# Kernel optimization log

Hardware: AMD Instinct MI355X
Metric: run time of the kernel (lower is better)

## Reference

```python
import jax, jax.numpy as jnp
import numpy as np

N_NODES = 100000
N_EDGES = 1600000
D_FEAT = 48


def sage_conv(x, src, dst, Wl, Wr, b):
    # mean aggregation of neighbor messages x[src] at dst (PyG source_to_target)
    msg_sum = jax.ops.segment_sum(x[src], dst, num_segments=N_NODES)  # [N, d]
    cnt = jax.ops.segment_sum(jnp.ones((src.shape[0],), x.dtype), dst,
                              num_segments=N_NODES)  # [N]
    mean = msg_sum / jnp.maximum(cnt, 1.0)[:, None]
    # out = lin_l(mean neighbors) + lin_r(self); bias only on lin_l (PyG default)
    return mean @ Wl + b + x @ Wr


def setup_inputs() -> dict:
    key = jax.random.key(0)
    ks = jax.random.split(key, 8)
    x = jax.random.normal(ks[0], (N_NODES, D_FEAT), jnp.float32)
    edge_index = jax.random.randint(ks[1], (2, N_EDGES), 0, N_NODES, jnp.int64)
    def w(k, fi, fo):
        return jax.random.normal(k, (fi, fo), jnp.float32) / np.sqrt(fi)
    return {
        "x": x,
        "edge_index": edge_index,
        "W1l": w(ks[2], D_FEAT, 32), "W1r": w(ks[3], D_FEAT, 32),
        "b1": jnp.zeros((32,), jnp.float32),
        "W2l": w(ks[4], 32, 16), "W2r": w(ks[5], 32, 16),
        "b2": jnp.zeros((16,), jnp.float32),
        "Wlin": w(ks[6], 16, 2), "blin": jnp.zeros((2,), jnp.float32),
    }


def reference(x, edge_index, W1l, W1r, b1, W2l, W2r, b2, Wlin, blin):
    src, dst = edge_index[0], edge_index[1]
    h = jax.nn.relu(sage_conv(x, src, dst, W1l, W1r, b1))
    h = jax.nn.relu(sage_conv(h, src, dst, W2l, W2r, b2))
    return h @ Wlin + blin  # [N, 2] logits
```

## Files before the change

kernel.cpp:

```cpp
#include <hip/hip_runtime.h>
#include <hip/hip_bf16.h>


constexpr int NN  = 100000;
constexpr int NE  = 1600000;
constexpr int NCH = (NN + 255) / 256;
constexpr int NB  = 391;
constexpr int CAP = 4608;
constexpr int SEG = CAP + 3 * 256;
constexpr int T1  = 2048;
constexpr int NB1 = (NE + T1 - 1) / T1;

__device__ __forceinline__ float bl(unsigned u) { return __uint_as_float(u << 16); }
__device__ __forceinline__ float bh(unsigned u) { return __uint_as_float(u & 0xffff0000u); }
__device__ __forceinline__ unsigned f2b(float x) {
    unsigned u = __float_as_uint(x);
    return (u + 0x7fffu + ((u >> 16) & 1u)) >> 16;
}
__device__ __forceinline__ unsigned pack2(float a, float b) {
    return f2b(a) | (f2b(b) << 16);
}

__device__ __forceinline__ int wave_incl_scan(int v, int lane) {
#pragma unroll
    for (int d = 1; d < 64; d <<= 1) {
        int t = __shfl_up(v, d, 64);
        if (lane >= d) v += t;
    }
    return v;
}

__global__ __launch_bounds__(256) void k1_kernel(
    const float* __restrict__ X,
    const float* __restrict__ Wl,
    const float* __restrict__ Wr,
    const int*   __restrict__ ei,
    int* __restrict__ bsize, unsigned* __restrict__ bbuf,
    __hip_bfloat16* __restrict__ P, __hip_bfloat16* __restrict__ R)
{
    __shared__ float sW[2][48 * 32];
    __shared__ int hist[NB], base[NB];
    __shared__ int s_any;

    if (blockIdx.x < NCH) {
        for (int i = threadIdx.x; i < 48 * 32; i += 256) {
            sW[0][i] = Wl[i];
            sW[1][i] = Wr[i];
        }
        __syncthreads();
        int n = blockIdx.x * 256 + threadIdx.x;
        if (n > NN) return;
        if (n == NN) {
            uint4 z = make_uint4(0, 0, 0, 0);
            uint4* pp = reinterpret_cast<uint4*>(P + (size_t)NN * 32);
#pragma unroll
            for (int i = 0; i < 4; ++i) pp[i] = z;
            return;
        }
        float xr[48];
        const float4* xp = reinterpret_cast<const float4*>(X + (size_t)n * 48);
#pragma unroll
        for (int i = 0; i < 12; ++i) {
            float4 u = xp[i];
            xr[i*4+0] = u.x; xr[i*4+1] = u.y; xr[i*4+2] = u.z; xr[i*4+3] = u.w;
        }
        float accp[32], accr[32];
#pragma unroll
        for (int j = 0; j < 32; ++j) { accp[j] = 0.f; accr[j] = 0.f; }
#pragma unroll
        for (int k = 0; k < 48; ++k) {
            float xk = xr[k];
#pragma unroll
            for (int j = 0; j < 32; ++j) {
                accp[j] += xk * sW[0][k * 32 + j];
                accr[j] += xk * sW[1][k * 32 + j];
            }
        }
        uint4* pp = reinterpret_cast<uint4*>(P + (size_t)n * 32);
        uint4* rp = reinterpret_cast<uint4*>(R + (size_t)n * 32);
#pragma unroll
        for (int i = 0; i < 4; ++i) {
            uint4 u, v;
            u.x = pack2(accp[i*8+0], accp[i*8+1]); u.y = pack2(accp[i*8+2], accp[i*8+3]);
            u.z = pack2(accp[i*8+4], accp[i*8+5]); u.w = pack2(accp[i*8+6], accp[i*8+7]);
            v.x = pack2(accr[i*8+0], accr[i*8+1]); v.y = pack2(accr[i*8+2], accr[i*8+3]);
            v.z = pack2(accr[i*8+4], accr[i*8+5]); v.w = pack2(accr[i*8+6], accr[i*8+7]);
            pp[i] = u;
            rp[i] = v;
        }
    } else {
        if (threadIdx.x == 0) s_any = 0;
        for (int i = threadIdx.x; i < NB; i += 256) hist[i] = 0;
        __syncthreads();
        int dv = 0;
        for (int i = threadIdx.x; i < 2048; i += 256) dv |= ei[2 * i + 1];
        if (dv != 0) atomicOr(&s_any, 1);
        __syncthreads();
        const bool i64 = (s_any == 0);
        const int e0 = (blockIdx.x - NCH) * T1;

        auto sweep = [&](auto&& f) {
            if (i64) {
                const int4* sp = reinterpret_cast<const int4*>(ei) + (e0 >> 1);
                const int4* dp = reinterpret_cast<const int4*>(ei) + ((NE + e0) >> 1);
#pragma unroll
                for (int it = 0; it < 4; ++it) {
                    int p = it * 256 + threadIdx.x;
                    int e = e0 + 2 * p;
                    if (e + 2 <= NE) {
                        int4 s4 = sp[p], d4 = dp[p];
                        f(s4.x, d4.x);
                        f(s4.z, d4.z);
                    } else {
                        for (int e2 = e; e2 < NE && e2 < e + 2; ++e2)
                            f(ei[(size_t)e2 << 1], ei[(size_t)(NE + e2) << 1]);
                    }
                }
            } else {
                const int4* sp = reinterpret_cast<const int4*>(ei) + (e0 >> 2);
                const int4* dp = reinterpret_cast<const int4*>(ei) + ((NE + e0) >> 2);
#pragma unroll
                for (int it = 0; it < 2; ++it) {
                    int q = it * 256 + threadIdx.x;
                    int e = e0 + 4 * q;
                    if (e + 4 <= NE) {
                        int4 s4 = sp[q], d4 = dp[q];
                        f(s4.x, d4.x);
                        f(s4.y, d4.y);
                        f(s4.z, d4.z);
                        f(s4.w, d4.w);
                    } else {
                        for (int e2 = e; e2 < NE && e2 < e + 4; ++e2)
                            f(ei[e2], ei[NE + e2]);
                    }
                }
            }
        };

        sweep([&](int s, int d) {
            if ((unsigned)s < (unsigned)NN && (unsigned)d < (unsigned)NN)
                atomicAdd(&hist[d >> 8], 1);
        });
        __syncthreads();
        for (int b = threadIdx.x; b < NB; b += 256) {
            int h = hist[b];
            base[b] = h ? atomicAdd(&bsize[b], h) : 0;
        }
        __syncthreads();
        sweep([&](int s, int d) {
            if ((unsigned)s < (unsigned)NN && (unsigned)d < (unsigned)NN) {
                int bk = d >> 8;
                int pos = atomicAdd(&base[bk], 1);
                if (pos < CAP)
                    bbuf[(size_t)bk * CAP + pos] =
                        ((unsigned)s << 8) | (unsigned)(d & 255);
            }
        });
    }
}

__global__ __launch_bounds__(1024) void k2_kernel(
    const int* __restrict__ bsize, const unsigned* __restrict__ bbuf,
    int* __restrict__ deg, int* __restrict__ rowstart, int* __restrict__ csr_src)
{
    __shared__ int ldeg[256], lcur[256], ws[4];
    int b = blockIdx.x, t = threadIdx.x;
    int bs = b * SEG;

    int S = min(bsize[b], CAP);
    const unsigned* bp = bbuf + (size_t)b * CAP;
    if (t < 256) ldeg[t] = 0;
    __syncthreads();
    for (int i = t; i < S; i += 1024)
        atomicAdd(&ldeg[bp[i] & 255u], 1);
    __syncthreads();

    int v = 0, pv = 0, incl = 0, excl = 0;
    if (t < 256) {
        v  = ldeg[t];
        pv = (v + 3) & ~3;
        incl = wave_incl_scan(pv, t & 63);
        if ((t & 63) == 63) ws[t >> 6] = incl;
    }
    __syncthreads();
    if (t < 256) {
        int off = 0, wid = t >> 6;
#pragma unroll
        for (int w = 0; w < 3; ++w)
            if (wid > w) off += ws[w];
        excl = off + incl - pv;
        int node = (b << 8) + t;
        if (node < NN) {
            deg[node] = v;
            rowstart[node] = bs + excl;
        }
        lcur[t] = excl;
    }
    __syncthreads();

    for (int i = t; i < S; i += 1024) {
        unsigned pk = bp[i];
        int pos = atomicAdd(&lcur[pk & 255u], 1);
        csr_src[bs + pos] = (int)(pk >> 8);
    }
    if (t < 256)
        for (int p = excl + v; p < excl + pv; ++p)
            csr_src[bs + p] = NN;
}

__global__ __launch_bounds__(256) void gather1f_kernel(
    const int* __restrict__ rowstart, const int* __restrict__ deg,
    const int* __restrict__ csr_src,
    const __hip_bfloat16* __restrict__ p1,
    const __hip_bfloat16* __restrict__ r1,
    const float* __restrict__ b1,
    const float* __restrict__ W2l,
    const float* __restrict__ W2r,
    __hip_bfloat16* __restrict__ P2,
    __hip_bfloat16* __restrict__ R2)
{
    __shared__ float sW2l[32 * 16], sW2r[32 * 16], sb1[32];
    __shared__ float shh[32 * 65];
    int t = threadIdx.x;
    for (int i = t; i < 32 * 16; i += 256) { sW2l[i] = W2l[i]; sW2r[i] = W2r[i]; }
    if (t < 32) sb1[t] = b1[t];
    __syncthreads();

    int loc = t >> 2, c = t & 3;
    int n = blockIdx.x * 64 + loc;
    bool valid = n < NN;

    if (valid) {
        int start = rowstart[n], dn = deg[n];
        int pv4 = ((dn + 3) & ~3) >> 2;
        const uint4* prow = reinterpret_cast<const uint4*>(p1);
        const int4* cp4 = reinterpret_cast<const int4*>(csr_src + start);
        uint4 r = reinterpret_cast<const uint4*>(r1)[(size_t)n * 4 + c];
        float acc[8];
#pragma unroll
        for (int j = 0; j < 8; ++j) acc[j] = 0.f;
        int k = 0;
        int4 sA = cp4[0];
        int4 sB = cp4[1];
        for (; k + 1 < pv4; k += 2) {
            int4 nA = cp4[k + 2];
            int4 nB = cp4[k + 3];
            uint4 a = prow[(size_t)sA.x * 4 + c];
            uint4 b = prow[(size_t)sA.y * 4 + c];
            uint4 d = prow[(size_t)sA.z * 4 + c];
            uint4 e = prow[(size_t)sA.w * 4 + c];
            uint4 f = prow[(size_t)sB.x * 4 + c];
            uint4 g = prow[(size_t)sB.y * 4 + c];
            uint4 h = prow[(size_t)sB.z * 4 + c];
            uint4 m = prow[(size_t)sB.w * 4 + c];
            acc[0] += bl(a.x) + bl(b.x) + bl(d.x) + bl(e.x)
                    + bl(f.x) + bl(g.x) + bl(h.x) + bl(m.x);
            acc[1] += bh(a.x) + bh(b.x) + bh(d.x) + bh(e.x)
                    + bh(f.x) + bh(g.x) + bh(h.x) + bh(m.x);
            acc[2] += bl(a.y) + bl(b.y) + bl(d.y) + bl(e.y)
                    + bl(f.y) + bl(g.y) + bl(h.y) + bl(m.y);
            acc[3] += bh(a.y) + bh(b.y) + bh(d.y) + bh(e.y)
                    + bh(f.y) + bh(g.y) + bh(h.y) + bh(m.y);
            acc[4] += bl(a.z) + bl(b.z) + bl(d.z) + bl(e.z)
                    + bl(f.z) + bl(g.z) + bl(h.z) + bl(m.z);
            acc[5] += bh(a.z) + bh(b.z) + bh(d.z) + bh(e.z)
                    + bh(f.z) + bh(g.z) + bh(h.z) + bh(m.z);
            acc[6] += bl(a.w) + bl(b.w) + bl(d.w) + bl(e.w)
                    + bl(f.w) + bl(g.w) + bl(h.w) + bl(m.w);
            acc[7] += bh(a.w) + bh(b.w) + bh(d.w) + bh(e.w)
                    + bh(f.w) + bh(g.w) + bh(h.w) + bh(m.w);
            sA = nA; sB = nB;
        }
        if (k < pv4) {
            uint4 a = prow[(size_t)sA.x * 4 + c];
            uint4 b = prow[(size_t)sA.y * 4 + c];
            uint4 d = prow[(size_t)sA.z * 4 + c];
            uint4 e = prow[(size_t)sA.w * 4 + c];
            acc[0] += bl(a.x) + bl(b.x) + bl(d.x) + bl(e.x);
            acc[1] += bh(a.x) + bh(b.x) + bh(d.x) + bh(e.x);
            acc[2] += bl(a.y) + bl(b.y) + bl(d.y) + bl(e.y);
            acc[3] += bh(a.y) + bh(b.y) + bh(d.y) + bh(e.y);
            acc[4] += bl(a.z) + bl(b.z) + bl(d.z) + bl(e.z);
            acc[5] += bh(a.z) + bh(b.z) + bh(d.z) + bh(e.z);
            acc[6] += bl(a.w) + bl(b.w) + bl(d.w) + bl(e.w);
            acc[7] += bh(a.w) + bh(b.w) + bh(d.w) + bh(e.w);
        }
        float inv = 1.0f / fmaxf((float)dn, 1.0f);
        float rr[8] = { bl(r.x), bh(r.x), bl(r.y), bh(r.y),
                        bl(r.z), bh(r.z), bl(r.w), bh(r.w) };
#pragma unroll
        for (int j = 0; j < 8; ++j)
            shh[(c * 8 + j) * 65 + loc] = fmaxf(acc[j] * inv + rr[j] + sb1[c * 8 + j], 0.f);
    }
    __syncthreads();

    if (valid) {
        float accp[4], accr[4];
#pragma unroll
        for (int j = 0; j < 4; ++j) { accp[j] = 0.f; accr[j] = 0.f; }
#pragma unroll
        for (int k2i = 0; k2i < 32; ++k2i) {
            float hk = shh[k2i * 65 + loc];
#pragma unroll
            for (int j = 0; j < 4; ++j) {
                accp[j] += hk * sW2l[k2i * 16 + c * 4 + j];
                accr[j] += hk * sW2r[k2i * 16 + c * 4 + j];
            }
        }
        uint2 up, ur;
        up.x = pack2(accp[0], accp[1]); up.y = pack2(accp[2], accp[3]);
        ur.x = pack2(accr[0], accr[1]); ur.y = pack2(accr[2], accr[3]);
        reinterpret_cast<uint2*>(P2)[(size_t)n * 4 + c] = up;
        reinterpret_cast<uint2*>(R2)[(size_t)n * 4 + c] = ur;
    } else if (n == NN) {
        uint2 z = make_uint2(0, 0);
        reinterpret_cast<uint2*>(P2)[(size_t)NN * 4 + c] = z;
        reinterpret_cast<uint2*>(R2)[(size_t)NN * 4 + c] = z;
    }
}

__global__ __launch_bounds__(256) void gather2_kernel(
    const int* __restrict__ rowstart, const int* __restrict__ deg,
    const int* __restrict__ csr_src,
    const __hip_bfloat16* __restrict__ P2,
    const __hip_bfloat16* __restrict__ R2,
    const float* __restrict__ b2,
    const float* __restrict__ Wlin,
    const float* __restrict__ blin,
    float* __restrict__ out)
{
    __shared__ float sb[16], sW[32], sbl[2];
    if (threadIdx.x < 16) sb[threadIdx.x] = b2[threadIdx.x];
    else if (threadIdx.x < 48) sW[threadIdx.x - 16] = Wlin[threadIdx.x - 16];
    else if (threadIdx.x < 50) sbl[threadIdx.x - 48] = blin[threadIdx.x - 48];
    __syncthreads();
    int t = blockIdx.x * 256 + threadIdx.x;
    int n = t >> 1, c = t & 1;
    if (n >= NN) return;
    int start = rowstart[n], dn = deg[n];
    int pv4 = ((dn + 3) & ~3) >> 2;

    const uint4* prow = reinterpret_cast<const uint4*>(P2);
    const int4* cp4 = reinterpret_cast<const int4*>(csr_src + start);
    uint4 r = reinterpret_cast<const uint4*>(R2)[(size_t)n * 2 + c];
    float acc[8];
#pragma unroll
    for (int j = 0; j < 8; ++j) acc[j] = 0.f;
    int k = 0;
    int4 sA = cp4[0];
    int4 sB = cp4[1];
    for (; k + 1 < pv4; k += 2) {
        int4 nA = cp4[k + 2];
        int4 nB = cp4[k + 3];
        uint4 a = prow[(size_t)sA.x * 2 + c];
        uint4 b = prow[(size_t)sA.y * 2 + c];
        uint4 d = prow[(size_t)sA.z * 2 + c];
        uint4 e = prow[(size_t)sA.w * 2 + c];
        uint4 f = prow[(size_t)sB.x * 2 + c];
        uint4 g = prow[(size_t)sB.y * 2 + c];
        uint4 h = prow[(size_t)sB.z * 2 + c];
        uint4 m = prow[(size_t)sB.w * 2 + c];
        acc[0] += bl(a.x) + bl(b.x) + bl(d.x) + bl(e.x)
                + bl(f.x) + bl(g.x) + bl(h.x) + bl(m.x);
        acc[1] += bh(a.x) + bh(b.x) + bh(d.x) + bh(e.x)
                + bh(f.x) + bh(g.x) + bh(h.x) + bh(m.x);
        acc[2] += bl(a.y) + bl(b.y) + bl(d.y) + bl(e.y)
                + bl(f.y) + bl(g.y) + bl(h.y) + bl(m.y);
        acc[3] += bh(a.y) + bh(b.y) + bh(d.y) + bh(e.y)
                + bh(f.y) + bh(g.y) + bh(h.y) + bh(m.y);
        acc[4] += bl(a.z) + bl(b.z) + bl(d.z) + bl(e.z)
                + bl(f.z) + bl(g.z) + bl(h.z) + bl(m.z);
        acc[5] += bh(a.z) + bh(b.z) + bh(d.z) + bh(e.z)
                + bh(f.z) + bh(g.z) + bh(h.z) + bh(m.z);
        acc[6] += bl(a.w) + bl(b.w) + bl(d.w) + bl(e.w)
                + bl(f.w) + bl(g.w) + bl(h.w) + bl(m.w);
        acc[7] += bh(a.w) + bh(b.w) + bh(d.w) + bh(e.w)
                + bh(f.w) + bh(g.w) + bh(h.w) + bh(m.w);
        sA = nA; sB = nB;
    }
    if (k < pv4) {
        uint4 a = prow[(size_t)sA.x * 2 + c];
        uint4 b = prow[(size_t)sA.y * 2 + c];
        uint4 d = prow[(size_t)sA.z * 2 + c];
        uint4 e = prow[(size_t)sA.w * 2 + c];
        acc[0] += bl(a.x) + bl(b.x) + bl(d.x) + bl(e.x);
        acc[1] += bh(a.x) + bh(b.x) + bh(d.x) + bh(e.x);
        acc[2] += bl(a.y) + bl(b.y) + bl(d.y) + bl(e.y);
        acc[3] += bh(a.y) + bh(b.y) + bh(d.y) + bh(e.y);
        acc[4] += bl(a.z) + bl(b.z) + bl(d.z) + bl(e.z);
        acc[5] += bh(a.z) + bh(b.z) + bh(d.z) + bh(e.z);
        acc[6] += bl(a.w) + bl(b.w) + bl(d.w) + bl(e.w);
        acc[7] += bh(a.w) + bh(b.w) + bh(d.w) + bh(e.w);
    }
    float inv = 1.0f / fmaxf((float)dn, 1.0f);
    float rr[8] = { bl(r.x), bh(r.x), bl(r.y), bh(r.y),
                    bl(r.z), bh(r.z), bl(r.w), bh(r.w) };
    float o0 = 0.f, o1 = 0.f;
#pragma unroll
    for (int j = 0; j < 8; ++j) {
        int kk = c * 8 + j;
        float hv = fmaxf(acc[j] * inv + rr[j] + sb[kk], 0.f);
        o0 += hv * sW[kk * 2];
        o1 += hv * sW[kk * 2 + 1];
    }
    o0 += __shfl_xor(o0, 1, 64);
    o1 += __shfl_xor(o1, 1, 64);
    if (c == 0)
        reinterpret_cast<float2*>(out)[n] = make_float2(o0 + sbl[0], o1 + sbl[1]);
}

extern "C" void kernel_launch(void* const* d_in, const int* in_sizes, int n_in,
                              void* d_out, int out_size, void* d_ws, size_t ws_size,
                              hipStream_t stream)
{
    const float* x    = (const float*)d_in[0];
    const int*   ei   = (const int*)d_in[1];
    const float* W1l  = (const float*)d_in[2];
    const float* W1r  = (const float*)d_in[3];
    const float* b1   = (const float*)d_in[4];
    const float* W2l  = (const float*)d_in[5];
    const float* W2r  = (const float*)d_in[6];
    const float* b2   = (const float*)d_in[7];
    const float* Wlin = (const float*)d_in[8];
    const float* blin = (const float*)d_in[9];
    float* out = (float*)d_out;

    char* wsb = (char*)d_ws;
    int*      bsize    = (int*)(wsb + 64);
    int*      deg      = (int*)(wsb + 4096);
    int*      rowstart = (int*)(wsb + 404096);
    int*      csr_src  = (int*)(wsb + 804096);
    unsigned* bbuf     = (unsigned*)(wsb + 9300000);
    __hip_bfloat16* p1 = (__hip_bfloat16*)(wsb + 16600000);
    __hip_bfloat16* r1 = (__hip_bfloat16*)(wsb + 23100000);
    __hip_bfloat16* p2 = (__hip_bfloat16*)(wsb + 29600000);
    __hip_bfloat16* r2 = (__hip_bfloat16*)(wsb + 32900000);

    dim3 blk(256);

    hipMemsetAsync(bsize, 0, NB * sizeof(int), stream);
    k1_kernel<<<NCH + NB1, blk, 0, stream>>>(x, W1l, W1r, ei, bsize, bbuf, p1, r1);
    k2_kernel<<<NB, dim3(1024), 0, stream>>>(bsize, bbuf, deg, rowstart, csr_src);
    gather1f_kernel<<<(NN + 1 + 63) / 64, blk, 0, stream>>>(
        rowstart, deg, csr_src, p1, r1, b1, W2l, W2r, p2, r2);
    gather2_kernel<<<(NN * 2 + 255) / 256, blk, 0, stream>>>(
        rowstart, deg, csr_src, p2, r2, b2, Wlin, blin, out);
}
```

Baseline: 175.9 us.

## Fuse CSR build into both gather kernels using shared-memory per-bucket CSR

Removes the separate k2 CSR-construction kernel and the global deg/rowstart/csr_src arrays. Each gather block now rebuilds its bucket's CSR in LDS from the bucketed edge buffer. Layer 1 uses half-buckets of 128 nodes per 512-thread block; layer 2 uses full 256-node buckets. This saves one launch and the global CSR write/read traffic. In exchange, the bucket is scanned twice (layer 2 reads it again and layer 1 filters each half), blocks are larger and use more LDS, and there are fewer blocks, which may lower occupancy for the latency-bound gathers.

```diff
diff --git a/kernel.cpp b/kernel.cpp
--- a/kernel.cpp
+++ b/kernel.cpp
@@ -8,6 +8,7 @@
 constexpr int NB  = 391;
 constexpr int CAP = 4608;
 constexpr int SEG = CAP + 3 * 256;
+constexpr int HSEG = CAP + 3 * 128;
 constexpr int T1  = 2048;
 constexpr int NB1 = (NE + T1 - 1) / T1;
 
@@ -159,58 +160,8 @@
     }
 }
 
-__global__ __launch_bounds__(1024) void k2_kernel(
+__global__ __launch_bounds__(512) void kg1_kernel(
     const int* __restrict__ bsize, const unsigned* __restrict__ bbuf,
-    int* __restrict__ deg, int* __restrict__ rowstart, int* __restrict__ csr_src)
-{
-    __shared__ int ldeg[256], lcur[256], ws[4];
-    int b = blockIdx.x, t = threadIdx.x;
-    int bs = b * SEG;
-
-    int S = min(bsize[b], CAP);
-    const unsigned* bp = bbuf + (size_t)b * CAP;
-    if (t < 256) ldeg[t] = 0;
-    __syncthreads();
-    for (int i = t; i < S; i += 1024)
-        atomicAdd(&ldeg[bp[i] & 255u], 1);
-    __syncthreads();
-
-    int v = 0, pv = 0, incl = 0, excl = 0;
-    if (t < 256) {
-        v  = ldeg[t];
-        pv = (v + 3) & ~3;
-        incl = wave_incl_scan(pv, t & 63);
-        if ((t & 63) == 63) ws[t >> 6] = incl;
-    }
-    __syncthreads();
-    if (t < 256) {
-        int off = 0, wid = t >> 6;
-#pragma unroll
-        for (int w = 0; w < 3; ++w)
-            if (wid > w) off += ws[w];
-        excl = off + incl - pv;
-        int node = (b << 8) + t;
-        if (node < NN) {
-            deg[node] = v;
-            rowstart[node] = bs + excl;
-        }
-        lcur[t] = excl;
-    }
-    __syncthreads();
-
-    for (int i = t; i < S; i += 1024) {
-        unsigned pk = bp[i];
-        int pos = atomicAdd(&lcur[pk & 255u], 1);
-        csr_src[bs + pos] = (int)(pk >> 8);
-    }
-    if (t < 256)
-        for (int p = excl + v; p < excl + pv; ++p)
-            csr_src[bs + p] = NN;
-}
-
-__global__ __launch_bounds__(256) void gather1f_kernel(
-    const int* __restrict__ rowstart, const int* __restrict__ deg,
-    const int* __restrict__ csr_src,
     const __hip_bfloat16* __restrict__ p1,
     const __hip_bfloat16* __restrict__ r1,
     const float* __restrict__ b1,
@@ -219,22 +170,66 @@
     __hip_bfloat16* __restrict__ P2,
     __hip_bfloat16* __restrict__ R2)
 {
+    __shared__ alignas(16) int csr[HSEG + 8];
+    __shared__ int ldeg[128], lcur[128], ws[2];
     __shared__ float sW2l[32 * 16], sW2r[32 * 16], sb1[32];
-    __shared__ float shh[32 * 65];
+    __shared__ float shh[32 * 129];
+
     int t = threadIdx.x;
-    for (int i = t; i < 32 * 16; i += 256) { sW2l[i] = W2l[i]; sW2r[i] = W2r[i]; }
+    int b = blockIdx.x >> 1, h = blockIdx.x & 1;
+
+    sW2l[t] = W2l[t];
+    sW2r[t] = W2r[t];
     if (t < 32) sb1[t] = b1[t];
+    if (t < 128) ldeg[t] = 0;
+    __syncthreads();
+
+    int S = min(bsize[b], CAP);
+    const unsigned* bp = bbuf + (size_t)b * CAP;
+    for (int i = t; i < S; i += 512) {
+        unsigned pk = bp[i];
+        int ln = pk & 255u;
+        if ((ln >> 7) == h) atomicAdd(&ldeg[ln & 127], 1);
+    }
+    __syncthreads();
+
+    int v = 0, pv = 0, incl = 0, excl = 0;
+    if (t < 128) {
+        v  = ldeg[t];
+        pv = (v + 3) & ~3;
+        incl = wave_incl_scan(pv, t & 63);
+        if ((t & 63) == 63) ws[t >> 6] = incl;
+    }
+    __syncthreads();
+    if (t < 128) {
+        int off = (t >> 6) ? ws[0] : 0;
+        excl = off + incl - pv;
+        lcur[t] = excl;
+    }
+    __syncthreads();
+    for (int i = t; i < S; i += 512) {
+        unsigned pk = bp[i];
+        int ln = pk & 255u;
+        if ((ln >> 7) == h) {
+            int pos = atomicAdd(&lcur[ln & 127], 1);
+            csr[pos] = (int)(pk >> 8);
+        }
+    }
+    if (t < 128)
+        for (int p = excl + v; p < excl + pv; ++p)
+            csr[p] = NN;
     __syncthreads();
 
     int loc = t >> 2, c = t & 3;
-    int n = blockIdx.x * 64 + loc;
+    int n = (b << 8) + (h << 7) + loc;
     bool valid = n < NN;
 
     if (valid) {
-        int start = rowstart[n], dn = deg[n];
+        int dn = ldeg[loc];
+        int start = lcur[loc] - dn;
         int pv4 = ((dn + 3) & ~3) >> 2;
         const uint4* prow = reinterpret_cast<const uint4*>(p1);
-        const int4* cp4 = reinterpret_cast<const int4*>(csr_src + start);
+        const int4* cp4 = reinterpret_cast<const int4*>(csr + start);
         uint4 r = reinterpret_cast<const uint4*>(r1)[(size_t)n * 4 + c];
         float acc[8];
 #pragma unroll
@@ -246,51 +241,51 @@
             int4 nA = cp4[k + 2];
             int4 nB = cp4[k + 3];
             uint4 a = prow[(size_t)sA.x * 4 + c];
-            uint4 b = prow[(size_t)sA.y * 4 + c];
+            uint4 bq = prow[(size_t)sA.y * 4 + c];
             uint4 d = prow[(size_t)sA.z * 4 + c];
             uint4 e = prow[(size_t)sA.w * 4 + c];
             uint4 f = prow[(size_t)sB.x * 4 + c];
             uint4 g = prow[(size_t)sB.y * 4 + c];
-            uint4 h = prow[(size_t)sB.z * 4 + c];
+            uint4 hq = prow[(size_t)sB.z * 4 + c];
             uint4 m = prow[(size_t)sB.w * 4 + c];
-            acc[0] += bl(a.x) + bl(b.x) + bl(d.x) + bl(e.x)
-                    + bl(f.x) + bl(g.x) + bl(h.x) + bl(m.x);
-            acc[1] += bh(a.x) + bh(b.x) + bh(d.x) + bh(e.x)
-                    + bh(f.x) + bh(g.x) + bh(h.x) + bh(m.x);
-            acc[2] += bl(a.y) + bl(b.y) + bl(d.y) + bl(e.y)
-                    + bl(f.y) + bl(g.y) + bl(h.y) + bl(m.y);
-            acc[3] += bh(a.y) + bh(b.y) + bh(d.y) + bh(e.y)
-                    + bh(f.y) + bh(g.y) + bh(h.y) + bh(m.y);
-            acc[4] += bl(a.z) + bl(b.z) + bl(d.z) + bl(e.z)
-                    + bl(f.z) + bl(g.z) + bl(h.z) + bl(m.z);
-            acc[5] += bh(a.z) + bh(b.z) + bh(d.z) + bh(e.z)
-                    + bh(f.z) + bh(g.z) + bh(h.z) + bh(m.z);
-            acc[6] += bl(a.w) + bl(b.w) + bl(d.w) + bl(e.w)
-                    + bl(f.w) + bl(g.w) + bl(h.w) + bl(m.w);
-            acc[7] += bh(a.w) + bh(b.w) + bh(d.w) + bh(e.w)
-                    + bh(f.w) + bh(g.w) + bh(h.w) + bh(m.w);
+            acc[0] += bl(a.x) + bl(bq.x) + bl(d.x) + bl(e.x)
+                    + bl(f.x) + bl(g.x) + bl(hq.x) + bl(m.x);
+            acc[1] += bh(a.x) + bh(bq.x) + bh(d.x) + bh(e.x)
+                    + bh(f.x) + bh(g.x) + bh(hq.x) + bh(m.x);
+            acc[2] += bl(a.y) + bl(bq.y) + bl(d.y) + bl(e.y)
+                    + bl(f.y) + bl(g.y) + bl(hq.y) + bl(m.y);
+            acc[3] += bh(a.y) + bh(bq.y) + bh(d.y) + bh(e.y)
+                    + bh(f.y) + bh(g.y) + bh(hq.y) + bh(m.y);
+            acc[4] += bl(a.z) + bl(bq.z) + bl(d.z) + bl(e.z)
+                    + bl(f.z) + bl(g.z) + bl(hq.z) + bl(m.z);
+            acc[5] += bh(a.z) + bh(bq.z) + bh(d.z) + bh(e.z)
+                    + bh(f.z) + bh(g.z) + bh(hq.z) + bh(m.z);
+            acc[6] += bl(a.w) + bl(bq.w) + bl(d.w) + bl(e.w)
+                    + bl(f.w) + bl(g.w) + bl(hq.w) + bl(m.w);
+            acc[7] += bh(a.w) + bh(bq.w) + bh(d.w) + bh(e.w)
+                    + bh(f.w) + bh(g.w) + bh(hq.w) + bh(m.w);
             sA = nA; sB = nB;
         }
         if (k < pv4) {
             uint4 a = prow[(size_t)sA.x * 4 + c];
-            uint4 b = prow[(size_t)sA.y * 4 + c];
+            uint4 bq = prow[(size_t)sA.y * 4 + c];
             uint4 d = prow[(size_t)sA.z * 4 + c];
             uint4 e = prow[(size_t)sA.w * 4 + c];
-            acc[0] += bl(a.x) + bl(b.x) + bl(d.x) + bl(e.x);
-            acc[1] += bh(a.x) + bh(b.x) + bh(d.x) + bh(e.x);
-            acc[2] += bl(a.y) + bl(b.y) + bl(d.y) + bl(e.y);
-            acc[3] += bh(a.y) + bh(b.y) + bh(d.y) + bh(e.y);
-            acc[4] += bl(a.z) + bl(b.z) + bl(d.z) + bl(e.z);
-            acc[5] += bh(a.z) + bh(b.z) + bh(d.z) + bh(e.z);
-            acc[6] += bl(a.w) + bl(b.w) + bl(d.w) + bl(e.w);
-            acc[7] += bh(a.w) + bh(b.w) + bh(d.w) + bh(e.w);
+            acc[0] += bl(a.x) + bl(bq.x) + bl(d.x) + bl(e.x);
+            acc[1] += bh(a.x) + bh(bq.x) + bh(d.x) + bh(e.x);
+            acc[2] += bl(a.y) + bl(bq.y) + bl(d.y) + bl(e.y);
+            acc[3] += bh(a.y) + bh(bq.y) + bh(d.y) + bh(e.y);
+            acc[4] += bl(a.z) + bl(bq.z) + bl(d.z) + bl(e.z);
+            acc[5] += bh(a.z) + bh(bq.z) + bh(d.z) + bh(e.z);
+            acc[6] += bl(a.w) + bl(bq.w) + bl(d.w) + bl(e.w);
+            acc[7] += bh(a.w) + bh(bq.w) + bh(d.w) + bh(e.w);
         }
         float inv = 1.0f / fmaxf((float)dn, 1.0f);
         float rr[8] = { bl(r.x), bh(r.x), bl(r.y), bh(r.y),
                         bl(r.z), bh(r.z), bl(r.w), bh(r.w) };
 #pragma unroll
         for (int j = 0; j < 8; ++j)
-            shh[(c * 8 + j) * 65 + loc] = fmaxf(acc[j] * inv + rr[j] + sb1[c * 8 + j], 0.f);
+            shh[(c * 8 + j) * 129 + loc] = fmaxf(acc[j] * inv + rr[j] + sb1[c * 8 + j], 0.f);
     }
     __syncthreads();
 
@@ -300,7 +295,7 @@
         for (int j = 0; j < 4; ++j) { accp[j] = 0.f; accr[j] = 0.f; }
 #pragma unroll
         for (int k2i = 0; k2i < 32; ++k2i) {
-            float hk = shh[k2i * 65 + loc];
+            float hk = shh[k2i * 129 + loc];
 #pragma unroll
             for (int j = 0; j < 4; ++j) {
                 accp[j] += hk * sW2l[k2i * 16 + c * 4 + j];
@@ -319,9 +314,8 @@
     }
 }
 
-__global__ __launch_bounds__(256) void gather2_kernel(
-    const int* __restrict__ rowstart, const int* __restrict__ deg,
-    const int* __restrict__ csr_src,
+__global__ __launch_bounds__(512) void kg2_kernel(
+    const int* __restrict__ bsize, const unsigned* __restrict__ bbuf,
     const __hip_bfloat16* __restrict__ P2,
     const __hip_bfloat16* __restrict__ R2,
     const float* __restrict__ b2,
@@ -329,19 +323,59 @@
     const float* __restrict__ blin,
     float* __restrict__ out)
 {
+    __shared__ alignas(16) int csr[SEG + 8];
+    __shared__ int ldeg[256], lcur[256], ws[4];
     __shared__ float sb[16], sW[32], sbl[2];
-    if (threadIdx.x < 16) sb[threadIdx.x] = b2[threadIdx.x];
-    else if (threadIdx.x < 48) sW[threadIdx.x - 16] = Wlin[threadIdx.x - 16];
-    else if (threadIdx.x < 50) sbl[threadIdx.x - 48] = blin[threadIdx.x - 48];
-    __syncthreads();
-    int t = blockIdx.x * 256 + threadIdx.x;
-    int n = t >> 1, c = t & 1;
+
+    int t = threadIdx.x, b = blockIdx.x;
+    if (t < 16) sb[t] = b2[t];
+    else if (t < 48) sW[t - 16] = Wlin[t - 16];
+    else if (t < 50) sbl[t - 48] = blin[t - 48];
+    if (t < 256) ldeg[t] = 0;
+    __syncthreads();
+
+    int S = min(bsize[b], CAP);
+    const unsigned* bp = bbuf + (size_t)b * CAP;
+    for (int i = t; i < S; i += 512)
+        atomicAdd(&ldeg[bp[i] & 255u], 1);
+    __syncthreads();
+
+    int v = 0, pv = 0, incl = 0, excl = 0;
+    if (t < 256) {
+        v  = ldeg[t];
+        pv = (v + 3) & ~3;
+        incl = wave_incl_scan(pv, t & 63);
+        if ((t & 63) == 63) ws[t >> 6] = incl;
+    }
+    __syncthreads();
+    if (t < 256) {
+        int off = 0, wid = t >> 6;
+#pragma unroll
+        for (int w = 0; w < 3; ++w)
+            if (wid > w) off += ws[w];
+        excl = off + incl - pv;
+        lcur[t] = excl;
+    }
+    __syncthreads();
+    for (int i = t; i < S; i += 512) {
+        unsigned pk = bp[i];
+        int pos = atomicAdd(&lcur[pk & 255u], 1);
+        csr[pos] = (int)(pk >> 8);
+    }
+    if (t < 256)
+        for (int p = excl + v; p < excl + pv; ++p)
+            csr[p] = NN;
+    __syncthreads();
+
+    int ln = t >> 1, c = t & 1;
+    int n = (b << 8) + ln;
     if (n >= NN) return;
-    int start = rowstart[n], dn = deg[n];
+    int dn = ldeg[ln];
+    int start = lcur[ln] - dn;
     int pv4 = ((dn + 3) & ~3) >> 2;
 
     const uint4* prow = reinterpret_cast<const uint4*>(P2);
-    const int4* cp4 = reinterpret_cast<const int4*>(csr_src + start);
+    const int4* cp4 = reinterpret_cast<const int4*>(csr + start);
     uint4 r = reinterpret_cast<const uint4*>(R2)[(size_t)n * 2 + c];
     float acc[8];
 #pragma unroll
@@ -353,44 +387,44 @@
         int4 nA = cp4[k + 2];
         int4 nB = cp4[k + 3];
         uint4 a = prow[(size_t)sA.x * 2 + c];
-        uint4 b = prow[(size_t)sA.y * 2 + c];
+        uint4 bq = prow[(size_t)sA.y * 2 + c];
         uint4 d = prow[(size_t)sA.z * 2 + c];
         uint4 e = prow[(size_t)sA.w * 2 + c];
         uint4 f = prow[(size_t)sB.x * 2 + c];
         uint4 g = prow[(size_t)sB.y * 2 + c];
         uint4 h = prow[(size_t)sB.z * 2 + c];
         uint4 m = prow[(size_t)sB.w * 2 + c];
-        acc[0] += bl(a.x) + bl(b.x) + bl(d.x) + bl(e.x)
+        acc[0] += bl(a.x) + bl(bq.x) + bl(d.x) + bl(e.x)
                 + bl(f.x) + bl(g.x) + bl(h.x) + bl(m.x);
-        acc[1] += bh(a.x) + bh(b.x) + bh(d.x) + bh(e.x)
+        acc[1] += bh(a.x) + bh(bq.x) + bh(d.x) + bh(e.x)
                 + bh(f.x) + bh(g.x) + bh(h.x) + bh(m.x);
-        acc[2] += bl(a.y) + bl(b.y) + bl(d.y) + bl(e.y)
+        acc[2] += bl(a.y) + bl(bq.y) + bl(d.y) + bl(e.y)
                 + bl(f.y) + bl(g.y) + bl(h.y) + bl(m.y);
-        acc[3] += bh(a.y) + bh(b.y) + bh(d.y) + bh(e.y)
+        acc[3] += bh(a.y) + bh(bq.y) + bh(d.y) + bh(e.y)
                 + bh(f.y) + bh(g.y) + bh(h.y) + bh(m.y);
-        acc[4] += bl(a.z) + bl(b.z) + bl(d.z) + bl(e.z)
+        acc[4] += bl(a.z) + bl(bq.z) + bl(d.z) + bl(e.z)
                 + bl(f.z) + bl(g.z) + bl(h.z) + bl(m.z);
-        acc[5] += bh(a.z) + bh(b.z) + bh(d.z) + bh(e.z)
+        acc[5] += bh(a.z) + bh(bq.z) + bh(d.z) + bh(e.z)
                 + bh(f.z) + bh(g.z) + bh(h.z) + bh(m.z);
-        acc[6] += bl(a.w) + bl(b.w) + bl(d.w) + bl(e.w)
+        acc[6] += bl(a.w) + bl(bq.w) + bl(d.w) + bl(e.w)
                 + bl(f.w) + bl(g.w) + bl(h.w) + bl(m.w);
-        acc[7] += bh(a.w) + bh(b.w) + bh(d.w) + bh(e.w)
+        acc[7] += bh(a.w) + bh(bq.w) + bh(d.w) + bh(e.w)
                 + bh(f.w) + bh(g.w) + bh(h.w) + bh(m.w);
         sA = nA; sB = nB;
     }
     if (k < pv4) {
         uint4 a = prow[(size_t)sA.x * 2 + c];
-        uint4 b = prow[(size_t)sA.y * 2 + c];
+        uint4 bq = prow[(size_t)sA.y * 2 + c];
         uint4 d = prow[(size_t)sA.z * 2 + c];
         uint4 e = prow[(size_t)sA.w * 2 + c];
-        acc[0] += bl(a.x) + bl(b.x) + bl(d.x) + bl(e.x);
-        acc[1] += bh(a.x) + bh(b.x) + bh(d.x) + bh(e.x);
-        acc[2] += bl(a.y) + bl(b.y) + bl(d.y) + bl(e.y);
-        acc[3] += bh(a.y) + bh(b.y) + bh(d.y) + bh(e.y);
-        acc[4] += bl(a.z) + bl(b.z) + bl(d.z) + bl(e.z);
-        acc[5] += bh(a.z) + bh(b.z) + bh(d.z) + bh(e.z);
-        acc[6] += bl(a.w) + bl(b.w) + bl(d.w) + bl(e.w);
-        acc[7] += bh(a.w) + bh(b.w) + bh(d.w) + bh(e.w);
+        acc[0] += bl(a.x) + bl(bq.x) + bl(d.x) + bl(e.x);
+        acc[1] += bh(a.x) + bh(bq.x) + bh(d.x) + bh(e.x);
+        acc[2] += bl(a.y) + bl(bq.y) + bl(d.y) + bl(e.y);
+        acc[3] += bh(a.y) + bh(bq.y) + bh(d.y) + bh(e.y);
+        acc[4] += bl(a.z) + bl(bq.z) + bl(d.z) + bl(e.z);
+        acc[5] += bh(a.z) + bh(bq.z) + bh(d.z) + bh(e.z);
+        acc[6] += bl(a.w) + bl(bq.w) + bl(d.w) + bl(e.w);
+        acc[7] += bh(a.w) + bh(bq.w) + bh(d.w) + bh(e.w);
     }
     float inv = 1.0f / fmaxf((float)dn, 1.0f);
     float rr[8] = { bl(r.x), bh(r.x), bl(r.y), bh(r.y),
@@ -427,9 +461,6 @@
 
     char* wsb = (char*)d_ws;
     int*      bsize    = (int*)(wsb + 64);
-    int*      deg      = (int*)(wsb + 4096);
-    int*      rowstart = (int*)(wsb + 404096);
-    int*      csr_src  = (int*)(wsb + 804096);
     unsigned* bbuf     = (unsigned*)(wsb + 9300000);
     __hip_bfloat16* p1 = (__hip_bfloat16*)(wsb + 16600000);
     __hip_bfloat16* r1 = (__hip_bfloat16*)(wsb + 23100000);
@@ -440,9 +471,8 @@
 
     hipMemsetAsync(bsize, 0, NB * sizeof(int), stream);
     k1_kernel<<<NCH + NB1, blk, 0, stream>>>(x, W1l, W1r, ei, bsize, bbuf, p1, r1);
-    k2_kernel<<<NB, dim3(1024), 0, stream>>>(bsize, bbuf, deg, rowstart, csr_src);
-    gather1f_kernel<<<(NN + 1 + 63) / 64, blk, 0, stream>>>(
-        rowstart, deg, csr_src, p1, r1, b1, W2l, W2r, p2, r2);
-    gather2_kernel<<<(NN * 2 + 255) / 256, blk, 0, stream>>>(
-        rowstart, deg, csr_src, p2, r2, b2, Wlin, blin, out);
-}
+    kg1_kernel<<<NB * 2, dim3(512), 0, stream>>>(
+        bsize, bbuf, p1, r1, b1, W2l, W2r, p2, r2);
+    kg2_kernel<<<NB, dim3(512), 0, stream>>>(
+        bsize, bbuf, p2, r2, b2, Wlin, blin, out);
+}
```

After: 177.5 us. About the same (+0.9%).

## Fuse CSR bucket build with layer-1 gather and split first-layer linear by weight

Applied to the files above, without the earlier changes.

The CSR construction kernel is merged with the layer-1 gather. Each 1024-thread block builds its 256-node segment's CSR in shared memory, gathers neighbors from it directly, and still writes the CSR out for layer 2. This removes one launch and a global round-trip of the CSR before gather 1. Separately, the first linear kernel now assigns Wl and Wr projections to different blocks, halving per-thread registers and doubling block count. The risks are only 391 large blocks in the fused kernel, which limits parallelism during the latency-bound gather, and heavy shared memory use.

```diff
diff --git a/kernel.cpp b/kernel.cpp
--- a/kernel.cpp
+++ b/kernel.cpp
@@ -4,7 +4,7 @@
 
 constexpr int NN  = 100000;
 constexpr int NE  = 1600000;
-constexpr int NCH = (NN + 255) / 256;
+constexpr int NLN = 391;
 constexpr int NB  = 391;
 constexpr int CAP = 4608;
 constexpr int SEG = CAP + 3 * 256;
@@ -38,23 +38,26 @@
     int* __restrict__ bsize, unsigned* __restrict__ bbuf,
     __hip_bfloat16* __restrict__ P, __hip_bfloat16* __restrict__ R)
 {
-    __shared__ float sW[2][48 * 32];
+    __shared__ float sW1[48 * 32];
     __shared__ int hist[NB], base[NB];
     __shared__ int s_any;
 
-    if (blockIdx.x < NCH) {
-        for (int i = threadIdx.x; i < 48 * 32; i += 256) {
-            sW[0][i] = Wl[i];
-            sW[1][i] = Wr[i];
-        }
+    if (blockIdx.x < 2 * NLN) {
+        const bool isP = blockIdx.x < NLN;
+        const float* W = isP ? Wl : Wr;
+        __hip_bfloat16* O = isP ? P : R;
+        for (int i = threadIdx.x; i < 48 * 32; i += 256)
+            sW1[i] = W[i];
         __syncthreads();
-        int n = blockIdx.x * 256 + threadIdx.x;
+        int n = (blockIdx.x - (isP ? 0 : NLN)) * 256 + threadIdx.x;
         if (n > NN) return;
         if (n == NN) {
-            uint4 z = make_uint4(0, 0, 0, 0);
-            uint4* pp = reinterpret_cast<uint4*>(P + (size_t)NN * 32);
-#pragma unroll
-            for (int i = 0; i < 4; ++i) pp[i] = z;
+            if (isP) {
+                uint4 z = make_uint4(0, 0, 0, 0);
+                uint4* pp = reinterpret_cast<uint4*>(P + (size_t)NN * 32);
+#pragma unroll
+                for (int i = 0; i < 4; ++i) pp[i] = z;
+            }
             return;
         }
         float xr[48];
@@ -64,29 +67,23 @@
             float4 u = xp[i];
             xr[i*4+0] = u.x; xr[i*4+1] = u.y; xr[i*4+2] = u.z; xr[i*4+3] = u.w;
         }
-        float accp[32], accr[32];
-#pragma unroll
-        for (int j = 0; j < 32; ++j) { accp[j] = 0.f; accr[j] = 0.f; }
+        float acc[32];
+#pragma unroll
+        for (int j = 0; j < 32; ++j) acc[j] = 0.f;
 #pragma unroll
         for (int k = 0; k < 48; ++k) {
             float xk = xr[k];
 #pragma unroll
-            for (int j = 0; j < 32; ++j) {
-                accp[j] += xk * sW[0][k * 32 + j];
-                accr[j] += xk * sW[1][k * 32 + j];
-            }
-        }
-        uint4* pp = reinterpret_cast<uint4*>(P + (size_t)n * 32);
-        uint4* rp = reinterpret_cast<uint4*>(R + (size_t)n * 32);
+            for (int j = 0; j < 32; ++j)
+                acc[j] += xk * sW1[k * 32 + j];
+        }
+        uint4* op = reinterpret_cast<uint4*>(O + (size_t)n * 32);
 #pragma unroll
         for (int i = 0; i < 4; ++i) {
-            uint4 u, v;
-            u.x = pack2(accp[i*8+0], accp[i*8+1]); u.y = pack2(accp[i*8+2], accp[i*8+3]);
-            u.z = pack2(accp[i*8+4], accp[i*8+5]); u.w = pack2(accp[i*8+6], accp[i*8+7]);
-            v.x = pack2(accr[i*8+0], accr[i*8+1]); v.y = pack2(accr[i*8+2], accr[i*8+3]);
-            v.z = pack2(accr[i*8+4], accr[i*8+5]); v.w = pack2(accr[i*8+6], accr[i*8+7]);
-            pp[i] = u;
-            rp[i] = v;
+            uint4 u;
+            u.x = pack2(acc[i*8+0], acc[i*8+1]); u.y = pack2(acc[i*8+2], acc[i*8+3]);
+            u.z = pack2(acc[i*8+4], acc[i*8+5]); u.w = pack2(acc[i*8+6], acc[i*8+7]);
+            op[i] = u;
         }
     } else {
         if (threadIdx.x == 0) s_any = 0;
@@ -97,7 +94,7 @@
         if (dv != 0) atomicOr(&s_any, 1);
         __syncthreads();
         const bool i64 = (s_any == 0);
-        const int e0 = (blockIdx.x - NCH) * T1;
+        const int e0 = (blockIdx.x - 2 * NLN) * T1;
 
         auto sweep = [&](auto&& f) {
             if (i64) {
@@ -159,18 +156,32 @@
     }
 }
 
-__global__ __launch_bounds__(1024) void k2_kernel(
+__global__ __launch_bounds__(1024) void kg1_kernel(
     const int* __restrict__ bsize, const unsigned* __restrict__ bbuf,
-    int* __restrict__ deg, int* __restrict__ rowstart, int* __restrict__ csr_src)
+    const __hip_bfloat16* __restrict__ p1,
+    const __hip_bfloat16* __restrict__ r1,
+    const float* __restrict__ b1,
+    const float* __restrict__ W2l,
+    const float* __restrict__ W2r,
+    int* __restrict__ csr_g,
+    int* __restrict__ deg_g,
+    int* __restrict__ rows_g,
+    __hip_bfloat16* __restrict__ P2,
+    __hip_bfloat16* __restrict__ R2)
 {
+    __shared__ alignas(16) int csr[SEG + 8];
     __shared__ int ldeg[256], lcur[256], ws[4];
-    int b = blockIdx.x, t = threadIdx.x;
-    int bs = b * SEG;
+    __shared__ float sW2l[32 * 16], sW2r[32 * 16], sb1[32];
+    __shared__ float shh[32 * 257];
+
+    int t = threadIdx.x, b = blockIdx.x;
+    if (t < 512) { sW2l[t] = W2l[t]; sW2r[t] = W2r[t]; }
+    else if (t < 544) sb1[t - 512] = b1[t - 512];
+    if (t < 256) ldeg[t] = 0;
+    __syncthreads();
 
     int S = min(bsize[b], CAP);
     const unsigned* bp = bbuf + (size_t)b * CAP;
-    if (t < 256) ldeg[t] = 0;
-    __syncthreads();
     for (int i = t; i < S; i += 1024)
         atomicAdd(&ldeg[bp[i] & 255u], 1);
     __syncthreads();
@@ -189,52 +200,35 @@
         for (int w = 0; w < 3; ++w)
             if (wid > w) off += ws[w];
         excl = off + incl - pv;
+        lcur[t] = excl;
         int node = (b << 8) + t;
         if (node < NN) {
-            deg[node] = v;
-            rowstart[node] = bs + excl;
-        }
-        lcur[t] = excl;
-    }
-    __syncthreads();
-
+            deg_g[node] = v;
+            rows_g[node] = b * SEG + excl;
+        }
+    }
+    __syncthreads();
     for (int i = t; i < S; i += 1024) {
         unsigned pk = bp[i];
         int pos = atomicAdd(&lcur[pk & 255u], 1);
-        csr_src[bs + pos] = (int)(pk >> 8);
+        csr[pos] = (int)(pk >> 8);
     }
     if (t < 256)
         for (int p = excl + v; p < excl + pv; ++p)
-            csr_src[bs + p] = NN;
-}
-
-__global__ __launch_bounds__(256) void gather1f_kernel(
-    const int* __restrict__ rowstart, const int* __restrict__ deg,
-    const int* __restrict__ csr_src,
-    const __hip_bfloat16* __restrict__ p1,
-    const __hip_bfloat16* __restrict__ r1,
-    const float* __restrict__ b1,
-    const float* __restrict__ W2l,
-    const float* __restrict__ W2r,
-    __hip_bfloat16* __restrict__ P2,
-    __hip_bfloat16* __restrict__ R2)
-{
-    __shared__ float sW2l[32 * 16], sW2r[32 * 16], sb1[32];
-    __shared__ float shh[32 * 65];
-    int t = threadIdx.x;
-    for (int i = t; i < 32 * 16; i += 256) { sW2l[i] = W2l[i]; sW2r[i] = W2r[i]; }
-    if (t < 32) sb1[t] = b1[t];
-    __syncthreads();
+            csr[p] = NN;
+    __syncthreads();
+
+    for (int p = t; p < SEG; p += 1024)
+        csr_g[b * SEG + p] = csr[p];
 
     int loc = t >> 2, c = t & 3;
-    int n = blockIdx.x * 64 + loc;
-    bool valid = n < NN;
-
-    if (valid) {
-        int start = rowstart[n], dn = deg[n];
+    int n = (b << 8) + loc;
+    if (n < NN) {
+        int dn = ldeg[loc];
+        int start = lcur[loc] - dn;
         int pv4 = ((dn + 3) & ~3) >> 2;
         const uint4* prow = reinterpret_cast<const uint4*>(p1);
-        const int4* cp4 = reinterpret_cast<const int4*>(csr_src + start);
+        const int4* cp4 = reinterpret_cast<const int4*>(csr + start);
         uint4 r = reinterpret_cast<const uint4*>(r1)[(size_t)n * 4 + c];
         float acc[8];
 #pragma unroll
@@ -246,61 +240,66 @@
             int4 nA = cp4[k + 2];
             int4 nB = cp4[k + 3];
             uint4 a = prow[(size_t)sA.x * 4 + c];
-            uint4 b = prow[(size_t)sA.y * 4 + c];
+            uint4 bq = prow[(size_t)sA.y * 4 + c];
             uint4 d = prow[(size_t)sA.z * 4 + c];
             uint4 e = prow[(size_t)sA.w * 4 + c];
             uint4 f = prow[(size_t)sB.x * 4 + c];
             uint4 g = prow[(size_t)sB.y * 4 + c];
-            uint4 h = prow[(size_t)sB.z * 4 + c];
+            uint4 hq = prow[(size_t)sB.z * 4 + c];
             uint4 m = prow[(size_t)sB.w * 4 + c];
-            acc[0] += bl(a.x) + bl(b.x) + bl(d.x) + bl(e.x)
-                    + bl(f.x) + bl(g.x) + bl(h.x) + bl(m.x);
-            acc[1] += bh(a.x) + bh(b.x) + bh(d.x) + bh(e.x)
-                    + bh(f.x) + bh(g.x) + bh(h.x) + bh(m.x);
-            acc[2] += bl(a.y) + bl(b.y) + bl(d.y) + bl(e.y)
-                    + bl(f.y) + bl(g.y) + bl(h.y) + bl(m.y);
-            acc[3] += bh(a.y) + bh(b.y) + bh(d.y) + bh(e.y)
-                    + bh(f.y) + bh(g.y) + bh(h.y) + bh(m.y);
-            acc[4] += bl(a.z) + bl(b.z) + bl(d.z) + bl(e.z)
-                    + bl(f.z) + bl(g.z) + bl(h.z) + bl(m.z);
-            acc[5] += bh(a.z) + bh(b.z) + bh(d.z) + bh(e.z)
-                    + bh(f.z) + bh(g.z) + bh(h.z) + bh(m.z);
-            acc[6] += bl(a.w) + bl(b.w) + bl(d.w) + bl(e.w)
-                    + bl(f.w) + bl(g.w) + bl(h.w) + bl(m.w);
-            acc[7] += bh(a.w) + bh(b.w) + bh(d.w) + bh(e.w)
-                    + bh(f.w) + bh(g.w) + bh(h.w) + bh(m.w);
+            acc[0] += bl(a.x) + bl(bq.x) + bl(d.x) + bl(e.x)
+                    + bl(f.x) + bl(g.x) + bl(hq.x) + bl(m.x);
+            acc[1] += bh(a.x) + bh(bq.x) + bh(d.x) + bh(e.x)
+                    + bh(f.x) + bh(g.x) + bh(hq.x) + bh(m.x);
+            acc[2] += bl(a.y) + bl(bq.y) + bl(d.y) + bl(e.y)
+                    + bl(f.y) + bl(g.y) + bl(hq.y) + bl(m.y);
+            acc[3] += bh(a.y) + bh(bq.y) + bh(d.y) + bh(e.y)
+                    + bh(f.y) + bh(g.y) + bh(hq.y) + bh(m.y);
+            acc[4] += bl(a.z) + bl(bq.z) + bl(d.z) + bl(e.z)
+                    + bl(f.z) + bl(g.z) + bl(hq.z) + bl(m.z);
+            acc[5] += bh(a.z) + bh(bq.z) + bh(d.z) + bh(e.z)
+                    + bh(f.z) + bh(g.z) + bh(hq.z) + bh(m.z);
+            acc[6] += bl(a.w) + bl(bq.w) + bl(d.w) + bl(e.w)
+                    + bl(f.w) + bl(g.w) + bl(hq.w) + bl(m.w);
+            acc[7] += bh(a.w) + bh(bq.w) + bh(d.w) + bh(e.w)
+                    + bh(f.w) + bh(g.w) + bh(hq.w) + bh(m.w);
             sA = nA; sB = nB;
         }
         if (k < pv4) {
             uint4 a = prow[(size_t)sA.x * 4 + c];
-            uint4 b = prow[(size_t)sA.y * 4 + c];
+            uint4 bq = prow[(size_t)sA.y * 4 + c];
             uint4 d = prow[(size_t)sA.z * 4 + c];
             uint4 e = prow[(size_t)sA.w * 4 + c];
-            acc[0] += bl(a.x) + bl(b.x) + bl(d.x) + bl(e.x);
-            acc[1] += bh(a.x) + bh(b.x) + bh(d.x) + bh(e.x);
-            acc[2] += bl(a.y) + bl(b.y) + bl(d.y) + bl(e.y);
-            acc[3] += bh(a.y) + bh(b.y) + bh(d.y) + bh(e.y);
-            acc[4] += bl(a.z) + bl(b.z) + bl(d.z) + bl(e.z);
-            acc[5] += bh(a.z) + bh(b.z) + bh(d.z) + bh(e.z);
-            acc[6] += bl(a.w) + bl(b.w) + bl(d.w) + bl(e.w);
-            acc[7] += bh(a.w) + bh(b.w) + bh(d.w) + bh(e.w);
+            acc[0] += bl(a.x) + bl(bq.x) + bl(d.x) + bl(e.x);
+            acc[1] += bh(a.x) + bh(bq.x) + bh(d.x) + bh(e.x);
+            acc[2] += bl(a.y) + bl(bq.y) + bl(d.y) + bl(e.y);
+            acc[3] += bh(a.y) + bh(bq.y) + bh(d.y) + bh(e.y);
+            acc[4] += bl(a.z) + bl(bq.z) + bl(d.z) + bl(e.z);
+            acc[5] += bh(a.z) + bh(bq.z) + bh(d.z) + bh(e.z);
+            acc[6] += bl(a.w) + bl(bq.w) + bl(d.w) + bl(e.w);
+            acc[7] += bh(a.w) + bh(bq.w) + bh(d.w) + bh(e.w);
         }
         float inv = 1.0f / fmaxf((float)dn, 1.0f);
         float rr[8] = { bl(r.x), bh(r.x), bl(r.y), bh(r.y),
                         bl(r.z), bh(r.z), bl(r.w), bh(r.w) };
 #pragma unroll
         for (int j = 0; j < 8; ++j)
-            shh[(c * 8 + j) * 65 + loc] = fmaxf(acc[j] * inv + rr[j] + sb1[c * 8 + j], 0.f);
-    }
-    __syncthreads();
-
-    if (valid) {
+            shh[(c * 8 + j) * 257 + loc] =
+                fmaxf(acc[j] * inv + rr[j] + sb1[c * 8 + j], 0.f);
+    } else if (n == NN) {
+        uint2 z = make_uint2(0, 0);
+        reinterpret_cast<uint2*>(P2)[(size_t)NN * 4 + c] = z;
+        reinterpret_cast<uint2*>(R2)[(size_t)NN * 4 + c] = z;
+    }
+    __syncthreads();
+
+    if (n < NN) {
         float accp[4], accr[4];
 #pragma unroll
         for (int j = 0; j < 4; ++j) { accp[j] = 0.f; accr[j] = 0.f; }
 #pragma unroll
         for (int k2i = 0; k2i < 32; ++k2i) {
-            float hk = shh[k2i * 65 + loc];
+            float hk = shh[k2i * 257 + loc];
 #pragma unroll
             for (int j = 0; j < 4; ++j) {
                 accp[j] += hk * sW2l[k2i * 16 + c * 4 + j];
@@ -312,10 +311,6 @@
         ur.x = pack2(accr[0], accr[1]); ur.y = pack2(accr[2], accr[3]);
         reinterpret_cast<uint2*>(P2)[(size_t)n * 4 + c] = up;
         reinterpret_cast<uint2*>(R2)[(size_t)n * 4 + c] = ur;
-    } else if (n == NN) {
-        uint2 z = make_uint2(0, 0);
-        reinterpret_cast<uint2*>(P2)[(size_t)NN * 4 + c] = z;
-        reinterpret_cast<uint2*>(R2)[(size_t)NN * 4 + c] = z;
     }
 }
 
@@ -429,20 +424,18 @@
     int*      bsize    = (int*)(wsb + 64);
     int*      deg      = (int*)(wsb + 4096);
     int*      rowstart = (int*)(wsb + 404096);
-    int*      csr_src  = (int*)(wsb + 804096);
+    int*      csr_g    = (int*)(wsb + 804096);
     unsigned* bbuf     = (unsigned*)(wsb + 9300000);
     __hip_bfloat16* p1 = (__hip_bfloat16*)(wsb + 16600000);
     __hip_bfloat16* r1 = (__hip_bfloat16*)(wsb + 23100000);
     __hip_bfloat16* p2 = (__hip_bfloat16*)(wsb + 29600000);
     __hip_bfloat16* r2 = (__hip_bfloat16*)(wsb + 32900000);
 
-    dim3 blk(256);
-
     hipMemsetAsync(bsize, 0, NB * sizeof(int), stream);
-    k1_kernel<<<NCH + NB1, blk, 0, stream>>>(x, W1l, W1r, ei, bsize, bbuf, p1, r1);
-    k2_kernel<<<NB, dim3(1024), 0, stream>>>(bsize, bbuf, deg, rowstart, csr_src);
-    gather1f_kernel<<<(NN + 1 + 63) / 64, blk, 0, stream>>>(
-        rowstart, deg, csr_src, p1, r1, b1, W2l, W2r, p2, r2);
-    gather2_kernel<<<(NN * 2 + 255) / 256, blk, 0, stream>>>(
-        rowstart, deg, csr_src, p2, r2, b2, Wlin, blin, out);
-}
+    k1_kernel<<<2 * NLN + NB1, dim3(256), 0, stream>>>(
+        x, W1l, W1r, ei, bsize, bbuf, p1, r1);
+    kg1_kernel<<<NB, dim3(1024), 0, stream>>>(
+        bsize, bbuf, p1, r1, b1, W2l, W2r, csr_g, deg, rowstart, p2, r2);
+    gather2_kernel<<<(NN * 2 + 255) / 256, dim3(256), 0, stream>>>(
+        rowstart, deg, csr_g, p2, r2, b2, Wlin, blin, out);
+}
```

New measurement: 173.5 us, median of 2. About the same (-1.3%).
